# Optimization experiments

Hardware: AMD Instinct MI355X
Metric: run time of the kernel (lower is better)

## Reference

```python
import jax, jax.numpy as jnp
import numpy as np

B, T, C = 64, 384, 256
NH, NKV = 4, 2
HD = C // NH            # 64
NREP = NH // NKV        # 2
NE, TOPK = 8, 2
HID = int(8 / 3 * C)    # 682
EPS_RMS = 1e-6


def _rope_tables(t_len):
    inv_freq = 1.0 / (10000.0 ** (np.arange(0, HD, 2, dtype=np.float32) / HD))
    t = np.arange(t_len, dtype=np.float32)
    freqs = np.outer(t, inv_freq)                      # [T, HD/2]
    emb = np.concatenate([freqs, freqs], axis=-1)      # [T, HD]
    return jnp.asarray(np.cos(emb)), jnp.asarray(np.sin(emb))


def _rotate_half(x):
    h = x.shape[-1] // 2
    return jnp.concatenate([-x[..., h:], x[..., :h]], axis=-1)


def _rmsnorm(v, w):
    return v * jax.lax.rsqrt(jnp.mean(v * v, axis=-1, keepdims=True) + EPS_RMS) * w


def setup_inputs() -> dict:
    key = jax.random.key(0)
    ks = jax.random.split(key, 10)
    s = lambda k, shape: (jax.random.normal(k, shape, jnp.float32) * 0.02)
    return {
        "x": jax.random.normal(ks[0], (B, T, C), jnp.float32),
        "ln1_w": jnp.ones((C,), jnp.float32),
        "ln2_w": jnp.ones((C,), jnp.float32),
        "wq": s(ks[1], (NH * HD, C)),
        "wk": s(ks[2], (NKV * HD, C)),
        "wv": s(ks[3], (NKV * HD, C)),
        "wo": s(ks[4], (C, C)),
        "router_w": s(ks[5], (NE, C)),
        "w1": s(ks[6], (NE, HID, C)),
        "w2": s(ks[7], (NE, C, HID)),
        "w3": s(ks[8], (NE, HID, C)),
    }


def reference(x, ln1_w, ln2_w, wq, wk, wv, wo, router_w, w1, w2, w3):
    Bx, Tx, Cx = x.shape
    # --- attention sub-block ---
    h = _rmsnorm(x, ln1_w)
    q = (h @ wq.T).reshape(Bx, Tx, NH, HD).transpose(0, 2, 1, 3)    # [B,H,T,D]
    k = (h @ wk.T).reshape(Bx, Tx, NKV, HD).transpose(0, 2, 1, 3)   # [B,KV,T,D]
    v = (h @ wv.T).reshape(Bx, Tx, NKV, HD).transpose(0, 2, 1, 3)
    cos, sin = _rope_tables(Tx)
    cos, sin = cos[None, None], sin[None, None]
    q = q * cos + _rotate_half(q) * sin
    k = k * cos + _rotate_half(k) * sin
    k = jnp.repeat(k, NREP, axis=1)   # GQA: expand kv heads
    v = jnp.repeat(v, NREP, axis=1)
    scores = jnp.einsum('bhtd,bhsd->bhts', q, k) / jnp.sqrt(jnp.float32(HD))
    causal = jnp.tril(jnp.ones((Tx, Tx), dtype=bool))
    scores = jnp.where(causal[None, None], scores, jnp.float32(-1e30))
    att = jax.nn.softmax(scores, axis=-1)
    y = jnp.einsum('bhts,bhsd->bhtd', att, v).transpose(0, 2, 1, 3).reshape(Bx, Tx, Cx)
    x = x + y @ wo.T

    # --- MoE sub-block ---
    flat = _rmsnorm(x, ln2_w).reshape(-1, Cx)                  # [N, C]
    probs = jax.nn.softmax(flat @ router_w.T, axis=-1)         # [N, NE]
    tp, ti = jax.lax.top_k(probs, TOPK)
    tp = tp / (jnp.sum(tp, axis=-1, keepdims=True) + 1e-9)
    # per-token per-expert combine weight (0 if not selected)
    weights = jnp.sum(tp[..., None] * jax.nn.one_hot(ti, NE, dtype=flat.dtype), axis=1)  # [N, NE]
    out = jnp.zeros_like(flat)
    for e in range(NE):  # small fixed expert count
        hh = jax.nn.silu(flat @ w1[e].T) * (flat @ w3[e].T)
        out = out + weights[:, e:e + 1] * (hh @ w2[e].T)
    return x + out.reshape(Bx, Tx, Cx)
```

## Files before the change

kernel.cpp:

```cpp
#include <hip/hip_runtime.h>
#include <hip/hip_bf16.h>
#include <math.h>

typedef unsigned short u16t;
typedef __bf16 bf16x8 __attribute__((ext_vector_type(8)));
typedef float f32x4 __attribute__((ext_vector_type(4)));

#define NBATCH 64
#define NT 384
#define NC 256
#define NHID 682
#define NHIDP 704
#define NTOK (NBATCH * NT)
#define NSLOT (2 * NTOK + 1024)

#define SB0 196
#define SB1 (SB0 + 512)
#define SB2 (SB1 + 256)
#define SB3 (SB2 + 5632)
#define SB4 (SB3 + 5632)
#define SB5 (SB4 + 48)

static __device__ __forceinline__ float bf2f(u16t u) { return __uint_as_float(((unsigned int)u) << 16); }
static __device__ __forceinline__ u16t f2bf(float f) { return __builtin_bit_cast(u16t, __float2bfloat16(f)); }

static __device__ __forceinline__ void gload16(const void* gp, void* lp) {
  __builtin_amdgcn_global_load_lds((const __attribute__((address_space(1))) void*)gp,
                                   (__attribute__((address_space(3))) void*)lp, 16, 0, 0);
}

static __device__ __forceinline__ void pipe_barrier_full() {
  asm volatile("s_waitcnt vmcnt(0) lgkmcnt(0)" ::: "memory");
  __builtin_amdgcn_s_barrier();
  asm volatile("" ::: "memory");
}


__global__ __launch_bounds__(256) void k_setup(const float* __restrict__ wq, const float* __restrict__ wk,
                                               const float* __restrict__ wv, const float* __restrict__ wo,
                                               const float* __restrict__ w1, const float* __restrict__ w2,
                                               const float* __restrict__ w3,
                                               int* __restrict__ tok, float* __restrict__ tokw,
                                               int* __restrict__ ctrl,
                                               u16t* __restrict__ wqkvb, u16t* __restrict__ wob,
                                               u16t* __restrict__ w1p, u16t* __restrict__ w3p,
                                               u16t* __restrict__ w2p, float* __restrict__ rtab) {
  int blk = blockIdx.x, t = threadIdx.x;
  if (blk < SB0) {
    int i = blk * 256 + t;
    tok[i] = -1; tokw[i] = 0.f;
    if (blk == 0 && t < 64) ctrl[t] = 0;
  } else if (blk < SB1) {
    int i = (blk - SB0) * 256 + t;
    int row = i >> 8, col = i & 255;
    float s = (row < 256) ? wq[(size_t)row * 256 + col]
            : (row < 384) ? wk[(size_t)(row - 256) * 256 + col]
                          : wv[(size_t)(row - 384) * 256 + col];
    wqkvb[i] = f2bf(s);
  } else if (blk < SB2) {
    int i = (blk - SB1) * 256 + t;
    wob[i] = f2bf(wo[i]);
  } else if (blk < SB3) {
    int idx = (blk - SB2) * 256 + t;
    int kcol = idx & 255; int tmp = idx >> 8; int nrow = tmp % NHIDP; int e = tmp / NHIDP;
    if (nrow < NHID) {
      size_t src = ((size_t)e * NHID + nrow) * NC + kcol;
      w1p[idx] = f2bf(w1[src]); w3p[idx] = f2bf(w3[src]);
    } else { w1p[idx] = 0; w3p[idx] = 0; }
  } else if (blk < SB4) {
    int idx = (blk - SB3) * 256 + t;
    int kcol = idx % NHIDP; int tmp = idx / NHIDP; int nrow = tmp & 255; int e = tmp >> 8;
    w2p[idx] = (kcol < NHID) ? f2bf(w2[((size_t)e * NC + nrow) * NHID + kcol]) : (u16t)0;
  } else {
    int i = (blk - SB4) * 256 + t;
    int tt = i >> 5, d = i & 31;
    float ang = (float)tt * powf(10000.f, -(float)d * (1.f / 32.f));
    float s, c; sincosf(ang, &s, &c);
    ((float2*)rtab)[i] = make_float2(c, s);
  }
}

__global__ __launch_bounds__(256) void k_rms(const float* __restrict__ xin,
                                             const float* __restrict__ wg,
                                             u16t* __restrict__ out) {
  int w = threadIdx.x >> 6, l = threadIdx.x & 63;
  int n = blockIdx.x * 4 + w;
  const float* xr = xin + (size_t)n * NC;
  float4 xa = *(const float4*)(xr + l * 4);
  float ssq = xa.x * xa.x + xa.y * xa.y + xa.z * xa.z + xa.w * xa.w;
  for (int d = 1; d < 64; d <<= 1) ssq += __shfl_xor(ssq, d, 64);
  float rs = rsqrtf(ssq * (1.f / 256.f) + 1e-6f);
  float4 wa = *(const float4*)(wg + l * 4);
  ushort4 o;
  o.x = f2bf(xa.x * rs * wa.x);
  o.y = f2bf(xa.y * rs * wa.y);
  o.z = f2bf(xa.z * rs * wa.z);
  o.w = f2bf(xa.w * rs * wa.w);
  *(ushort4*)(out + (size_t)n * NC + l * 4) = o;
}

__global__ __launch_bounds__(256) void k_rms_router(const float* __restrict__ xin,
                                                    const float* __restrict__ wg,
                                                    const float* __restrict__ rw,
                                                    u16t* __restrict__ flat,
                                                    int* __restrict__ eidx,
                                                    float* __restrict__ ew) {
  int w = threadIdx.x >> 6, l = threadIdx.x & 63;
  int n = blockIdx.x * 4 + w;
  const float* xr = xin + (size_t)n * NC;
  float4 xa = *(const float4*)(xr + l * 4);
  float ssq = xa.x * xa.x + xa.y * xa.y + xa.z * xa.z + xa.w * xa.w;
  for (int d = 1; d < 64; d <<= 1) ssq += __shfl_xor(ssq, d, 64);
  float rs = rsqrtf(ssq * (1.f / 256.f) + 1e-6f);
  float4 wa = *(const float4*)(wg + l * 4);
  float n0 = xa.x * rs * wa.x, n1 = xa.y * rs * wa.y;
  float n2 = xa.z * rs * wa.z, n3 = xa.w * rs * wa.w;
  ushort4 o; o.x = f2bf(n0); o.y = f2bf(n1); o.z = f2bf(n2); o.w = f2bf(n3);
  *(ushort4*)(flat + (size_t)n * NC + l * 4) = o;
  float acc[8];
  for (int e = 0; e < 8; e++) {
    float4 ra = *(const float4*)(rw + (size_t)e * NC + l * 4);
    acc[e] = n0 * ra.x + n1 * ra.y + n2 * ra.z + n3 * ra.w;
  }
  for (int e = 0; e < 8; e++)
    for (int d = 1; d < 64; d <<= 1) acc[e] += __shfl_xor(acc[e], d, 64);
  if (l == 0) {
    float mx = acc[0];
    for (int e = 1; e < 8; e++) mx = fmaxf(mx, acc[e]);
    float p[8], sum = 0.f;
    for (int e = 0; e < 8; e++) { p[e] = __expf(acc[e] - mx); sum += p[e]; }
    float inv = 1.f / sum;
    for (int e = 0; e < 8; e++) p[e] *= inv;
    int i0 = 0; float b0 = p[0];
    for (int e = 1; e < 8; e++) if (p[e] > b0) { b0 = p[e]; i0 = e; }
    int i1 = -1; float b1 = -1.f;
    for (int e = 0; e < 8; e++) if (e != i0 && p[e] > b1) { b1 = p[e]; i1 = e; }
    float s2 = 1.f / (b0 + b1 + 1e-9f);
    eidx[n * 2] = i0; eidx[n * 2 + 1] = i1;
    ew[n * 2] = b0 * s2; ew[n * 2 + 1] = b1 * s2;
  }
}

__global__ __launch_bounds__(256) void k_hist(const int* __restrict__ eidx, int* __restrict__ ctrl) {
  int* cnt = ctrl; int* offs = ctrl + 8; int* cursor = ctrl + 20; int* done = ctrl + 32;
  __shared__ int lh[8];
  if (threadIdx.x < 8) lh[threadIdx.x] = 0;
  __syncthreads();
  int base = blockIdx.x * 1024 + threadIdx.x;
  for (int i = 0; i < 4; i++) atomicAdd(&lh[eidx[base + i * 256]], 1);
  __syncthreads();
  if (threadIdx.x < 8) {
    atomicAdd(&cnt[threadIdx.x], lh[threadIdx.x]);
    __threadfence();
  }
  __syncthreads();
  if (threadIdx.x == 0) {
    int prev = atomicAdd(done, 1);
    if (prev == 47) {
      int off = 0;
      for (int e = 0; e < 8; e++) {
        int c_ = atomicAdd(&cnt[e], 0);
        offs[e] = off; cursor[e] = off;
        off += ((c_ + 127) >> 7) << 7;
      }
      offs[8] = off;
    }
  }
}

__global__ __launch_bounds__(256) void k_gemm_qkv(const u16t* __restrict__ A,
                                                  const u16t* __restrict__ Bw,
                                                  const float* __restrict__ rtab,
                                                  u16t* __restrict__ qkv) {
  __shared__ __align__(16) u16t sA[2][128 * 64];
  __shared__ __align__(16) u16t sB[2][128 * 64];
  int t = threadIdx.x;
  int m0 = blockIdx.y * 128, n0 = blockIdx.x * 128;
  int w = t >> 6, l = t & 63, quad = l >> 4, lq = l & 15;
  int wm = (w >> 1) * 64, wn = (w & 1) * 64;
  const u16t* aP[4]; const u16t* bP[4];
  for (int i = 0; i < 4; i++) {
    int c = i * 256 + t; int r = c >> 3; int g = (c & 7) ^ (r & 7);
    aP[i] = A + (size_t)(m0 + r) * NC + g * 8;
    bP[i] = Bw + (size_t)(n0 + r) * NC + g * 8;
  }
  auto stage = [&](int p, int k0) {
    for (int i = 0; i < 4; i++) {
      gload16(aP[i] + k0, sA[p] + (size_t)(i * 256 + t) * 8);
      gload16(bP[i] + k0, sB[p] + (size_t)(i * 256 + t) * 8);
    }
  };
  const f32x4 fz = {0.f, 0.f, 0.f, 0.f};
  f32x4 acc[4][4];
  for (int i = 0; i < 4; i++) for (int j = 0; j < 4; j++) acc[i][j] = fz;
  stage(0, 0);
  pipe_barrier_full();
  for (int kb = 0; kb < 4; kb++) {
    int p = kb & 1;
    if (kb < 3) stage(p ^ 1, (kb + 1) << 6);
    for (int kk = 0; kk < 2; kk++) {
      int gq = kk * 4 + quad;
      bf16x8 af[4], bf[4];
      for (int mi = 0; mi < 4; mi++) { int row = wm + mi * 16 + lq; af[mi] = *(const bf16x8*)(sA[p] + (row * 8 + (gq ^ (row & 7))) * 8); }
      for (int ni = 0; ni < 4; ni++) { int row = wn + ni * 16 + lq; bf[ni] = *(const bf16x8*)(sB[p] + (row * 8 + (gq ^ (row & 7))) * 8); }
      for (int mi = 0; mi < 4; mi++)
        for (int ni = 0; ni < 4; ni++)
          acc[mi][ni] = __builtin_amdgcn_mfma_f32_16x16x32_bf16(af[mi], bf[ni], acc[mi][ni], 0, 0, 0);
    }
    if (kb < 3) pipe_barrier_full();
  }
  int cb = (n0 + wn) >> 6;
  const float2* rt = (const float2*)rtab;
  for (int mi = 0; mi < 4; mi++)
    for (int r = 0; r < 4; r++) {
      int gm = m0 + wm + mi * 16 + quad * 4 + r;
      u16t* orow = qkv + (size_t)gm * 512 + n0 + wn;
      if (cb < 6) {
        int tt = gm % NT;
        for (int ni = 0; ni < 2; ni++) {
          int d = ni * 16 + lq;
          float2 cs = rt[tt * 32 + d];
          float x1 = acc[mi][ni][r], x2 = acc[mi][ni + 2][r];
          orow[d] = f2bf(x1 * cs.x - x2 * cs.y);
          orow[d + 32] = f2bf(x2 * cs.x + x1 * cs.y);
        }
      } else {
        for (int ni = 0; ni < 4; ni++) orow[ni * 16 + lq] = f2bf(acc[mi][ni][r]);
      }
    }
}

__global__ __launch_bounds__(256) void k_gemm_wo(const u16t* __restrict__ A,
                                                 const u16t* __restrict__ Bw,
                                                 const float* __restrict__ xin,
                                                 float* __restrict__ xo) {
  __shared__ __align__(16) u16t sA[2][128 * 64];
  __shared__ __align__(16) u16t sB[2][128 * 64];
  int t = threadIdx.x;
  int m0 = blockIdx.y * 128, n0 = blockIdx.x * 128;
  int w = t >> 6, l = t & 63, quad = l >> 4, lq = l & 15;
  int wm = (w >> 1) * 64, wn = (w & 1) * 64;
  const u16t* aP[4]; const u16t* bP[4];
  for (int i = 0; i < 4; i++) {
    int c = i * 256 + t; int r = c >> 3; int g = (c & 7) ^ (r & 7);
    aP[i] = A + (size_t)(m0 + r) * NC + g * 8;
    bP[i] = Bw + (size_t)(n0 + r) * NC + g * 8;
  }
  auto stage = [&](int p, int k0) {
    for (int i = 0; i < 4; i++) {
      gload16(aP[i] + k0, sA[p] + (size_t)(i * 256 + t) * 8);
      gload16(bP[i] + k0, sB[p] + (size_t)(i * 256 + t) * 8);
    }
  };
  const f32x4 fz = {0.f, 0.f, 0.f, 0.f};
  f32x4 acc[4][4];
  for (int i = 0; i < 4; i++) for (int j = 0; j < 4; j++) acc[i][j] = fz;
  stage(0, 0);
  pipe_barrier_full();
  for (int kb = 0; kb < 4; kb++) {
    int p = kb & 1;
    if (kb < 3) stage(p ^ 1, (kb + 1) << 6);
    for (int kk = 0; kk < 2; kk++) {
      int gq = kk * 4 + quad;
      bf16x8 af[4], bf[4];
      for (int mi = 0; mi < 4; mi++) { int row = wm + mi * 16 + lq; af[mi] = *(const bf16x8*)(sA[p] + (row * 8 + (gq ^ (row & 7))) * 8); }
      for (int ni = 0; ni < 4; ni++) { int row = wn + ni * 16 + lq; bf[ni] = *(const bf16x8*)(sB[p] + (row * 8 + (gq ^ (row & 7))) * 8); }
      for (int mi = 0; mi < 4; mi++)
        for (int ni = 0; ni < 4; ni++)
          acc[mi][ni] = __builtin_amdgcn_mfma_f32_16x16x32_bf16(af[mi], bf[ni], acc[mi][ni], 0, 0, 0);
    }
    if (kb < 3) pipe_barrier_full();
  }
  for (int mi = 0; mi < 4; mi++)
    for (int ni = 0; ni < 4; ni++) {
      int gn = n0 + wn + ni * 16 + lq;
      for (int r = 0; r < 4; r++) {
        int gm = m0 + wm + mi * 16 + quad * 4 + r;
        xo[(size_t)gm * NC + gn] = acc[mi][ni][r] + xin[(size_t)gm * NC + gn];
      }
    }
}

__global__ __launch_bounds__(256) void k_attn(const u16t* __restrict__ qkv,
                                              u16t* __restrict__ y) {
  __shared__ __align__(16) u16t sK[2][64 * 64];
  __shared__ __align__(16) u16t sVT[2][64 * 64];
  __shared__ __align__(16) u16t sP[4 * 32 * 64];
  int qt = blockIdx.x, h = blockIdx.y, b = blockIdx.z;
  int kvh = h >> 1;
  int t = threadIdx.x, w = t >> 6, l = t & 63, quad = l >> 4, lq = l & 15;
  int tb = qt * 128 + w * 32;
  bf16x8 qf[2][2];
  for (int mi = 0; mi < 2; mi++)
    for (int kk = 0; kk < 2; kk++)
      qf[mi][kk] = *(const bf16x8*)(qkv + ((size_t)(b * NT + tb + mi * 16 + lq)) * 512 + h * 64 + kk * 32 + quad * 8);
  const f32x4 fz = {0.f, 0.f, 0.f, 0.f};
  f32x4 accO[2][4];
  float mrow[2][4], lrow[2][4];
  for (int mi = 0; mi < 2; mi++)
    for (int ni = 0; ni < 4; ni++) accO[mi][ni] = fz;
  for (int mi = 0; mi < 2; mi++)
    for (int r = 0; r < 4; r++) { mrow[mi][r] = -1e30f; lrow[mi][r] = 0.f; }
  u16t* myP = sP + w * 2048;
  int nkt = (qt + 1) * 2;
  ushort4 vr0[2], vr1[2];
  auto stageK = [&](int p, int kt) {
    int s0 = kt * 64;
    for (int i = 0; i < 2; i++) {
      int c = i * 256 + t; int s = c >> 3; int g = (c & 7) ^ (s & 7);
      gload16(qkv + ((size_t)(b * NT + s0 + s)) * 512 + 256 + kvh * 64 + g * 8, sK[p] + (size_t)c * 8);
    }
  };
  auto vload = [&](int kt) {
    int s0 = kt * 64;
    for (int i = 0; i < 2; i++) {
      int pI = i * 256 + t; int s = pI & 63; int n0 = (pI >> 6) * 8;
      const u16t* vp = qkv + ((size_t)(b * NT + s0 + s)) * 512 + 384 + kvh * 64 + n0;
      vr0[i] = *(const ushort4*)vp; vr1[i] = *(const ushort4*)(vp + 4);
    }
  };
  auto vstore = [&](int p) {
    for (int i = 0; i < 2; i++) {
      int pI = i * 256 + t; int s = pI & 63; int n0 = (pI >> 6) * 8;
      u16t vv[8] = {vr0[i].x, vr0[i].y, vr0[i].z, vr0[i].w, vr1[i].x, vr1[i].y, vr1[i].z, vr1[i].w};
      for (int j = 0; j < 8; j++) {
        int nn = n0 + j;
        sVT[p][(nn * 8 + ((s >> 3) ^ (nn & 7))) * 8 + (s & 7)] = vv[j];
      }
    }
  };
  stageK(0, 0); vload(0); vstore(0);
  pipe_barrier_full();
  for (int kt = 0; kt < nkt; kt++) {
    int p = kt & 1;
    int s0 = kt * 64;
    bool more = (kt + 1 < nkt);
    if (more) { stageK(p ^ 1, kt + 1); vload(kt + 1); }
    if (s0 <= tb + 31) {
      f32x4 accS[2][4];
      for (int mi = 0; mi < 2; mi++) for (int ni = 0; ni < 4; ni++) accS[mi][ni] = fz;
      for (int kk = 0; kk < 2; kk++) {
        int gq = kk * 4 + quad;
        bf16x8 kf[4];
        for (int ni = 0; ni < 4; ni++) { int row = ni * 16 + lq; kf[ni] = *(const bf16x8*)(sK[p] + (row * 8 + (gq ^ (row & 7))) * 8); }
        for (int mi = 0; mi < 2; mi++)
          for (int ni = 0; ni < 4; ni++)
            accS[mi][ni] = __builtin_amdgcn_mfma_f32_16x16x32_bf16(qf[mi][kk], kf[ni], accS[mi][ni], 0, 0, 0);
      }
      for (int mi = 0; mi < 2; mi++) {
        float alpha[4];
        for (int r = 0; r < 4; r++) {
          int trow = tb + mi * 16 + quad * 4 + r;
          float mx = -1e30f;
          for (int ni = 0; ni < 4; ni++) {
            int ss = s0 + ni * 16 + lq;
            float sv = accS[mi][ni][r] * 0.125f;
            sv = (ss > trow) ? -1e30f : sv;
            accS[mi][ni][r] = sv;
            mx = fmaxf(mx, sv);
          }
          for (int d = 1; d < 16; d <<= 1) mx = fmaxf(mx, __shfl_xor(mx, d, 64));
          float mnew = fmaxf(mrow[mi][r], mx);
          float al = __expf(mrow[mi][r] - mnew);
          float rsum = 0.f;
          for (int ni = 0; ni < 4; ni++) {
            float p2 = __expf(accS[mi][ni][r] - mnew);
            accS[mi][ni][r] = p2;
            rsum += p2;
          }
          for (int d = 1; d < 16; d <<= 1) rsum += __shfl_xor(rsum, d, 64);
          lrow[mi][r] = lrow[mi][r] * al + rsum;
          mrow[mi][r] = mnew;
          alpha[r] = al;
        }
        for (int ni = 0; ni < 4; ni++)
          for (int r = 0; r < 4; r++) accO[mi][ni][r] *= alpha[r];
        for (int ni = 0; ni < 4; ni++) {
          int cc = ni * 16 + lq;
          for (int r = 0; r < 4; r++) {
            int row = mi * 16 + quad * 4 + r;
            myP[((cc >> 3) * 32 + row) * 8 + (cc & 7)] = f2bf(accS[mi][ni][r]);
          }
        }
      }
      asm volatile("s_waitcnt lgkmcnt(0)" ::: "memory");
      for (int kk = 0; kk < 2; kk++) {
        int gq = kk * 4 + quad;
        bf16x8 pf[2], vf[4];
        for (int mi = 0; mi < 2; mi++) { int row = mi * 16 + lq; pf[mi] = *(const bf16x8*)(myP + (gq * 32 + row) * 8); }
        for (int ni = 0; ni < 4; ni++) { int row = ni * 16 + lq; vf[ni] = *(const bf16x8*)(sVT[p] + (row * 8 + (gq ^ (row & 7))) * 8); }
        for (int mi = 0; mi < 2; mi++)
          for (int ni = 0; ni < 4; ni++)
            accO[mi][ni] = __builtin_amdgcn_mfma_f32_16x16x32_bf16(pf[mi], vf[ni], accO[mi][ni], 0, 0, 0);
      }
    }
    if (more) {
      vstore(p ^ 1);
      pipe_barrier_full();
    }
  }
  for (int mi = 0; mi < 2; mi++)
    for (int r = 0; r < 4; r++) {
      int trow = tb + mi * 16 + quad * 4 + r;
      float inv = 1.f / lrow[mi][r];
      for (int ni = 0; ni < 4; ni++) {
        int d = ni * 16 + lq;
        y[((size_t)(b * NT + trow)) * NC + h * 64 + d] = f2bf(accO[mi][ni][r] * inv);
      }
    }
}

__global__ __launch_bounds__(256) void k_scatter(const int* __restrict__ eidx, const float* __restrict__ ew,
                                                 int* __restrict__ cursor, int* __restrict__ tok,
                                                 float* __restrict__ tokw, int* __restrict__ t2s) {
  __shared__ int lcnt[8], lbase[8];
  if (threadIdx.x < 8) lcnt[threadIdx.x] = 0;
  __syncthreads();
  int n = blockIdx.x * 256 + threadIdx.x;
  int e0 = eidx[n * 2], e1 = eidx[n * 2 + 1];
  int p0 = atomicAdd(&lcnt[e0], 1);
  int p1 = atomicAdd(&lcnt[e1], 1);
  __syncthreads();
  if (threadIdx.x < 8) lbase[threadIdx.x] = atomicAdd(&cursor[threadIdx.x], lcnt[threadIdx.x]);
  __syncthreads();
  int g0 = lbase[e0] + p0, g1 = lbase[e1] + p1;
  tok[g0] = n; tokw[g0] = ew[n * 2];
  tok[g1] = n; tokw[g1] = ew[n * 2 + 1];
  t2s[n * 2] = g0; t2s[n * 2 + 1] = g1;
}

__global__ __launch_bounds__(256) void k_moe_e1(const u16t* __restrict__ flat,
                                                const u16t* __restrict__ w1p,
                                                const u16t* __restrict__ w3p,
                                                const int* __restrict__ offs,
                                                const int* __restrict__ tok,
                                                u16t* __restrict__ hh) {
  __shared__ __align__(16) u16t sA[2][128 * 64];
  __shared__ __align__(16) u16t sB1[2][64 * 64];
  __shared__ __align__(16) u16t sB3[2][64 * 64];
  int t = threadIdx.x;
  int bid = blockIdx.x;
  int work = (bid & 7) * 539 + (bid >> 3);
  int sb = work / 11;
  int slot0 = sb * 128, n0 = (work - sb * 11) * 64;
  int e = 7;
  for (int i = 0; i < 8; i++) { if (slot0 < offs[i + 1]) { e = i; break; } }
  const u16t* B1 = w1p + (size_t)e * NHIDP * NC;
  const u16t* B3 = w3p + (size_t)e * NHIDP * NC;
  int w = t >> 6, l = t & 63, quad = l >> 4, lq = l & 15;
  int wm = (w >> 1) * 64, wn = (w & 1) * 32;
  const u16t* aP[4]; const u16t* b1P[2]; const u16t* b3P[2];
  for (int i = 0; i < 4; i++) {
    int c = i * 256 + t; int r = c >> 3; int g = (c & 7) ^ (r & 7);
    int tk = tok[slot0 + r]; int row = (tk < 0) ? 0 : tk;
    aP[i] = flat + (size_t)row * NC + g * 8;
  }
  for (int i = 0; i < 2; i++) {
    int c = i * 256 + t; int r = c >> 3; int g = (c & 7) ^ (r & 7);
    b1P[i] = B1 + (size_t)(n0 + r) * NC + g * 8;
    b3P[i] = B3 + (size_t)(n0 + r) * NC + g * 8;
  }
  auto stage = [&](int p, int k0) {
    for (int i = 0; i < 4; i++)
      gload16(aP[i] + k0, sA[p] + (size_t)(i * 256 + t) * 8);
    for (int i = 0; i < 2; i++) {
      gload16(b1P[i] + k0, sB1[p] + (size_t)(i * 256 + t) * 8);
      gload16(b3P[i] + k0, sB3[p] + (size_t)(i * 256 + t) * 8);
    }
  };
  const f32x4 fz = {0.f, 0.f, 0.f, 0.f};
  f32x4 a1[4][2], a3[4][2];
  for (int i = 0; i < 4; i++) for (int j = 0; j < 2; j++) { a1[i][j] = fz; a3[i][j] = fz; }
  stage(0, 0);
  pipe_barrier_full();
  for (int kb = 0; kb < 4; kb++) {
    int p = kb & 1;
    if (kb < 3) stage(p ^ 1, (kb + 1) << 6);
    for (int kk = 0; kk < 2; kk++) {
      int gq = kk * 4 + quad;
      bf16x8 af[4], b1f[2], b3f[2];
      for (int mi = 0; mi < 4; mi++) { int row = wm + mi * 16 + lq; af[mi] = *(const bf16x8*)(sA[p] + (row * 8 + (gq ^ (row & 7))) * 8); }
      for (int ni = 0; ni < 2; ni++) {
        int row = wn + ni * 16 + lq;
        b1f[ni] = *(const bf16x8*)(sB1[p] + (row * 8 + (gq ^ (row & 7))) * 8);
        b3f[ni] = *(const bf16x8*)(sB3[p] + (row * 8 + (gq ^ (row & 7))) * 8);
      }
      for (int mi = 0; mi < 4; mi++)
        for (int ni = 0; ni < 2; ni++) {
          a1[mi][ni] = __builtin_amdgcn_mfma_f32_16x16x32_bf16(af[mi], b1f[ni], a1[mi][ni], 0, 0, 0);
          a3[mi][ni] = __builtin_amdgcn_mfma_f32_16x16x32_bf16(af[mi], b3f[ni], a3[mi][ni], 0, 0, 0);
        }
    }
    if (kb < 3) pipe_barrier_full();
  }
  for (int mi = 0; mi < 4; mi++)
    for (int ni = 0; ni < 2; ni++) {
      int gn = n0 + wn + ni * 16 + lq;
      for (int r = 0; r < 4; r++) {
        int slot = slot0 + wm + mi * 16 + quad * 4 + r;
        float v1 = a1[mi][ni][r], v3 = a3[mi][ni][r];
        float hv = v1 / (1.f + __expf(-v1)) * v3;
        hh[(size_t)slot * NHIDP + gn] = f2bf(hv);
      }
    }
}

__global__ __launch_bounds__(256) void k_moe_e2(const u16t* __restrict__ hh,
                                                const u16t* __restrict__ w2p,
                                                const int* __restrict__ offs,
                                                const float* __restrict__ tokw,
                                                u16t* __restrict__ eo) {
  __shared__ __align__(16) u16t sA[2][128 * 64];
  __shared__ __align__(16) u16t sB[2][128 * 64];
  int t = threadIdx.x;
  int bid = blockIdx.x;
  int work = (bid & 7) * 98 + (bid >> 3);
  int slot0 = (work >> 1) * 128, n0 = (work & 1) * 128;
  int e = 7;
  for (int i = 0; i < 8; i++) { if (slot0 < offs[i + 1]) { e = i; break; } }
  const u16t* Bw = w2p + (size_t)e * NC * NHIDP;
  int w = t >> 6, l = t & 63, quad = l >> 4, lq = l & 15;
  int wm = (w >> 1) * 64, wn = (w & 1) * 64;
  const u16t* aP[4]; const u16t* bP[4];
  for (int i = 0; i < 4; i++) {
    int c = i * 256 + t; int r = c >> 3; int g = (c & 7) ^ (r & 7);
    aP[i] = hh + (size_t)(slot0 + r) * NHIDP + g * 8;
    bP[i] = Bw + (size_t)(n0 + r) * NHIDP + g * 8;
  }
  auto stage = [&](int p, int k0) {
    for (int i = 0; i < 4; i++) {
      gload16(aP[i] + k0, sA[p] + (size_t)(i * 256 + t) * 8);
      gload16(bP[i] + k0, sB[p] + (size_t)(i * 256 + t) * 8);
    }
  };
  const f32x4 fz = {0.f, 0.f, 0.f, 0.f};
  f32x4 acc[4][4];
  for (int i = 0; i < 4; i++) for (int j = 0; j < 4; j++) acc[i][j] = fz;
  stage(0, 0);
  pipe_barrier_full();
  for (int kb = 0; kb < 11; kb++) {
    int p = kb & 1;
    if (kb < 10) stage(p ^ 1, (kb + 1) << 6);
    for (int kk = 0; kk < 2; kk++) {
      int gq = kk * 4 + quad;
      bf16x8 af[4], bf[4];
      for (int mi = 0; mi < 4; mi++) { int row = wm + mi * 16 + lq; af[mi] = *(const bf16x8*)(sA[p] + (row * 8 + (gq ^ (row & 7))) * 8); }
      for (int ni = 0; ni < 4; ni++) { int row = wn + ni * 16 + lq; bf[ni] = *(const bf16x8*)(sB[p] + (row * 8 + (gq ^ (row & 7))) * 8); }
      for (int mi = 0; mi < 4; mi++)
        for (int ni = 0; ni < 4; ni++)
          acc[mi][ni] = __builtin_amdgcn_mfma_f32_16x16x32_bf16(af[mi], bf[ni], acc[mi][ni], 0, 0, 0);
    }
    if (kb < 10) pipe_barrier_full();
  }
  for (int mi = 0; mi < 4; mi++)
    for (int r = 0; r < 4; r++) {
      int slot = slot0 + wm + mi * 16 + quad * 4 + r;
      float wgt = tokw[slot];
      for (int ni = 0; ni < 4; ni++) {
        int gn = n0 + wn + ni * 16 + lq;
        eo[(size_t)slot * NC + gn] = f2bf(wgt * acc[mi][ni][r]);
      }
    }
}

__global__ __launch_bounds__(256) void k_combine(const u16t* __restrict__ eo,
                                                 const int* __restrict__ t2s,
                                                 float* __restrict__ xo) {
  int w = threadIdx.x >> 6, l = threadIdx.x & 63;
  int n = blockIdx.x * 4 + w;
  int g0 = t2s[n * 2], g1 = t2s[n * 2 + 1];
  float* xr = xo + (size_t)n * NC + l * 4;
  float4 xa = *(const float4*)xr;
  ushort4 a = *(const ushort4*)(eo + (size_t)g0 * NC + l * 4);
  ushort4 b = *(const ushort4*)(eo + (size_t)g1 * NC + l * 4);
  xa.x += bf2f(a.x) + bf2f(b.x);
  xa.y += bf2f(a.y) + bf2f(b.y);
  xa.z += bf2f(a.z) + bf2f(b.z);
  xa.w += bf2f(a.w) + bf2f(b.w);
  *(float4*)xr = xa;
}

extern "C" void kernel_launch(void* const* d_in, const int* in_sizes, int n_in,
                              void* d_out, int out_size, void* d_ws, size_t ws_size,
                              hipStream_t stream) {
  (void)in_sizes; (void)n_in; (void)out_size; (void)ws_size;
  const float* x    = (const float*)d_in[0];
  const float* ln1w = (const float*)d_in[1];
  const float* ln2w = (const float*)d_in[2];
  const float* wq   = (const float*)d_in[3];
  const float* wk   = (const float*)d_in[4];
  const float* wv   = (const float*)d_in[5];
  const float* wo   = (const float*)d_in[6];
  const float* rw   = (const float*)d_in[7];
  const float* w1   = (const float*)d_in[8];
  const float* w2   = (const float*)d_in[9];
  const float* w3   = (const float*)d_in[10];
  float* xo = (float*)d_out;

  char* ws = (char*)d_ws;
  size_t off = 0;
  int* ctrl  = (int*)(ws + off);  off += 4096;
  int* eidx  = (int*)(ws + off);  off += (size_t)NTOK * 2 * 4;
  float* ew  = (float*)(ws + off); off += (size_t)NTOK * 2 * 4;
  int* tok   = (int*)(ws + off);  off += (size_t)NSLOT * 4;
  float* tokw = (float*)(ws + off); off += (size_t)NSLOT * 4;
  int* t2s   = (int*)(ws + off);  off += (size_t)NTOK * 2 * 4;
  u16t* wqkvb = (u16t*)(ws + off); off += (size_t)512 * 256 * 2;
  u16t* wob  = (u16t*)(ws + off); off += (size_t)256 * 256 * 2;
  u16t* w1p  = (u16t*)(ws + off); off += (size_t)8 * NHIDP * NC * 2;
  u16t* w3p  = (u16t*)(ws + off); off += (size_t)8 * NHIDP * NC * 2;
  u16t* w2p  = (u16t*)(ws + off); off += (size_t)8 * NC * NHIDP * 2;
  float* rtab = (float*)(ws + off); off += (size_t)NT * 32 * 2 * 4;
  u16t* h    = (u16t*)(ws + off); off += (size_t)NTOK * NC * 2;
  u16t* qkv  = (u16t*)(ws + off); off += (size_t)NTOK * 512 * 2;
  u16t* y    = (u16t*)(ws + off); off += (size_t)NTOK * NC * 2;
  u16t* flat = (u16t*)(ws + off); off += (size_t)NTOK * NC * 2;
  u16t* hh   = (u16t*)(ws + off); off += (size_t)NSLOT * NHIDP * 2;
  u16t* eo   = h;
  int* offs = ctrl + 8; int* cursor = ctrl + 20;

  k_setup<<<SB5, 256, 0, stream>>>(wq, wk, wv, wo, w1, w2, w3,
                                   tok, tokw, ctrl, wqkvb, wob, w1p, w3p, w2p, rtab);
  k_rms<<<NTOK / 4, 256, 0, stream>>>(x, ln1w, h);
  k_gemm_qkv<<<dim3(4, NTOK / 128), 256, 0, stream>>>(h, wqkvb, rtab, qkv);
  k_attn<<<dim3(3, 4, NBATCH), 256, 0, stream>>>(qkv, y);
  k_gemm_wo<<<dim3(2, NTOK / 128), 256, 0, stream>>>(y, wob, x, xo);

  k_rms_router<<<NTOK / 4, 256, 0, stream>>>(xo, ln2w, rw, flat, eidx, ew);
  k_hist<<<48, 256, 0, stream>>>(eidx, ctrl);
  k_scatter<<<NTOK / 256, 256, 0, stream>>>(eidx, ew, cursor, tok, tokw, t2s);
  k_moe_e1<<<4312, 256, 0, stream>>>(flat, w1p, w3p, offs, tok, hh);
  k_moe_e2<<<784, 256, 0, stream>>>(hh, w2p, offs, tokw, eo);
  k_combine<<<NTOK / 4, 256, 0, stream>>>(eo, t2s, xo);
}
```

Measured before the change: 306.7 us.

## Single-buffer MoE GEMM LDS, raise MFMA priority, fold first RMSNorm into setup

The two MoE expert GEMM kernels drop LDS double buffering. Each K step now loads, syncs, computes and syncs again, which halves shared memory per block so more blocks can be resident. MFMA sections are wrapped in s_setprio to favour math waves. The first RMSNorm is merged into the setup kernel as extra blocks, removing one launch. The trade-off is that global loads no longer overlap compute within a block, so the kernel relies on occupancy to hide latency.

```diff
diff --git a/kernel.cpp b/kernel.cpp
--- a/kernel.cpp
+++ b/kernel.cpp
@@ -20,6 +20,7 @@
 #define SB3 (SB2 + 5632)
 #define SB4 (SB3 + 5632)
 #define SB5 (SB4 + 48)
+#define SB6 (SB5 + NTOK / 4)
 
 static __device__ __forceinline__ float bf2f(u16t u) { return __uint_as_float(((unsigned int)u) << 16); }
 static __device__ __forceinline__ u16t f2bf(float f) { return __builtin_bit_cast(u16t, __float2bfloat16(f)); }
@@ -40,11 +41,13 @@
                                                const float* __restrict__ wv, const float* __restrict__ wo,
                                                const float* __restrict__ w1, const float* __restrict__ w2,
                                                const float* __restrict__ w3,
+                                               const float* __restrict__ x, const float* __restrict__ ln1w,
                                                int* __restrict__ tok, float* __restrict__ tokw,
                                                int* __restrict__ ctrl,
                                                u16t* __restrict__ wqkvb, u16t* __restrict__ wob,
                                                u16t* __restrict__ w1p, u16t* __restrict__ w3p,
-                                               u16t* __restrict__ w2p, float* __restrict__ rtab) {
+                                               u16t* __restrict__ w2p, float* __restrict__ rtab,
+                                               u16t* __restrict__ h) {
   int blk = blockIdx.x, t = threadIdx.x;
   if (blk < SB0) {
     int i = blk * 256 + t;
@@ -71,32 +74,28 @@
     int idx = (blk - SB3) * 256 + t;
     int kcol = idx % NHIDP; int tmp = idx / NHIDP; int nrow = tmp & 255; int e = tmp >> 8;
     w2p[idx] = (kcol < NHID) ? f2bf(w2[((size_t)e * NC + nrow) * NHID + kcol]) : (u16t)0;
-  } else {
+  } else if (blk < SB5) {
     int i = (blk - SB4) * 256 + t;
     int tt = i >> 5, d = i & 31;
     float ang = (float)tt * powf(10000.f, -(float)d * (1.f / 32.f));
     float s, c; sincosf(ang, &s, &c);
     ((float2*)rtab)[i] = make_float2(c, s);
-  }
-}
-
-__global__ __launch_bounds__(256) void k_rms(const float* __restrict__ xin,
-                                             const float* __restrict__ wg,
-                                             u16t* __restrict__ out) {
-  int w = threadIdx.x >> 6, l = threadIdx.x & 63;
-  int n = blockIdx.x * 4 + w;
-  const float* xr = xin + (size_t)n * NC;
-  float4 xa = *(const float4*)(xr + l * 4);
-  float ssq = xa.x * xa.x + xa.y * xa.y + xa.z * xa.z + xa.w * xa.w;
-  for (int d = 1; d < 64; d <<= 1) ssq += __shfl_xor(ssq, d, 64);
-  float rs = rsqrtf(ssq * (1.f / 256.f) + 1e-6f);
-  float4 wa = *(const float4*)(wg + l * 4);
-  ushort4 o;
-  o.x = f2bf(xa.x * rs * wa.x);
-  o.y = f2bf(xa.y * rs * wa.y);
-  o.z = f2bf(xa.z * rs * wa.z);
-  o.w = f2bf(xa.w * rs * wa.w);
-  *(ushort4*)(out + (size_t)n * NC + l * 4) = o;
+  } else {
+    int w = t >> 6, l = t & 63;
+    int n = (blk - SB5) * 4 + w;
+    const float* xr = x + (size_t)n * NC;
+    float4 xa = *(const float4*)(xr + l * 4);
+    float ssq = xa.x * xa.x + xa.y * xa.y + xa.z * xa.z + xa.w * xa.w;
+    for (int d = 1; d < 64; d <<= 1) ssq += __shfl_xor(ssq, d, 64);
+    float rs = rsqrtf(ssq * (1.f / 256.f) + 1e-6f);
+    float4 wa = *(const float4*)(ln1w + l * 4);
+    ushort4 o;
+    o.x = f2bf(xa.x * rs * wa.x);
+    o.y = f2bf(xa.y * rs * wa.y);
+    o.z = f2bf(xa.z * rs * wa.z);
+    o.w = f2bf(xa.w * rs * wa.w);
+    *(ushort4*)(h + (size_t)n * NC + l * 4) = o;
+  }
 }
 
 __global__ __launch_bounds__(256) void k_rms_router(const float* __restrict__ xin,
@@ -435,9 +434,9 @@
                                                 const int* __restrict__ offs,
                                                 const int* __restrict__ tok,
                                                 u16t* __restrict__ hh) {
-  __shared__ __align__(16) u16t sA[2][128 * 64];
-  __shared__ __align__(16) u16t sB1[2][64 * 64];
-  __shared__ __align__(16) u16t sB3[2][64 * 64];
+  __shared__ __align__(16) u16t sA[128 * 64];
+  __shared__ __align__(16) u16t sB1[64 * 64];
+  __shared__ __align__(16) u16t sB3[64 * 64];
   int t = threadIdx.x;
   int bid = blockIdx.x;
   int work = (bid & 7) * 539 + (bid >> 3);
@@ -460,38 +459,36 @@
     b1P[i] = B1 + (size_t)(n0 + r) * NC + g * 8;
     b3P[i] = B3 + (size_t)(n0 + r) * NC + g * 8;
   }
-  auto stage = [&](int p, int k0) {
-    for (int i = 0; i < 4; i++)
-      gload16(aP[i] + k0, sA[p] + (size_t)(i * 256 + t) * 8);
-    for (int i = 0; i < 2; i++) {
-      gload16(b1P[i] + k0, sB1[p] + (size_t)(i * 256 + t) * 8);
-      gload16(b3P[i] + k0, sB3[p] + (size_t)(i * 256 + t) * 8);
-    }
-  };
   const f32x4 fz = {0.f, 0.f, 0.f, 0.f};
   f32x4 a1[4][2], a3[4][2];
   for (int i = 0; i < 4; i++) for (int j = 0; j < 2; j++) { a1[i][j] = fz; a3[i][j] = fz; }
-  stage(0, 0);
-  pipe_barrier_full();
   for (int kb = 0; kb < 4; kb++) {
-    int p = kb & 1;
-    if (kb < 3) stage(p ^ 1, (kb + 1) << 6);
+    int k0 = kb << 6;
+    for (int i = 0; i < 4; i++)
+      gload16(aP[i] + k0, sA + (size_t)(i * 256 + t) * 8);
+    for (int i = 0; i < 2; i++) {
+      gload16(b1P[i] + k0, sB1 + (size_t)(i * 256 + t) * 8);
+      gload16(b3P[i] + k0, sB3 + (size_t)(i * 256 + t) * 8);
+    }
+    __syncthreads();
     for (int kk = 0; kk < 2; kk++) {
       int gq = kk * 4 + quad;
       bf16x8 af[4], b1f[2], b3f[2];
-      for (int mi = 0; mi < 4; mi++) { int row = wm + mi * 16 + lq; af[mi] = *(const bf16x8*)(sA[p] + (row * 8 + (gq ^ (row & 7))) * 8); }
+      for (int mi = 0; mi < 4; mi++) { int row = wm + mi * 16 + lq; af[mi] = *(const bf16x8*)(sA + (row * 8 + (gq ^ (row & 7))) * 8); }
       for (int ni = 0; ni < 2; ni++) {
         int row = wn + ni * 16 + lq;
-        b1f[ni] = *(const bf16x8*)(sB1[p] + (row * 8 + (gq ^ (row & 7))) * 8);
-        b3f[ni] = *(const bf16x8*)(sB3[p] + (row * 8 + (gq ^ (row & 7))) * 8);
-      }
+        b1f[ni] = *(const bf16x8*)(sB1 + (row * 8 + (gq ^ (row & 7))) * 8);
+        b3f[ni] = *(const bf16x8*)(sB3 + (row * 8 + (gq ^ (row & 7))) * 8);
+      }
+      __builtin_amdgcn_s_setprio(1);
       for (int mi = 0; mi < 4; mi++)
         for (int ni = 0; ni < 2; ni++) {
           a1[mi][ni] = __builtin_amdgcn_mfma_f32_16x16x32_bf16(af[mi], b1f[ni], a1[mi][ni], 0, 0, 0);
           a3[mi][ni] = __builtin_amdgcn_mfma_f32_16x16x32_bf16(af[mi], b3f[ni], a3[mi][ni], 0, 0, 0);
         }
-    }
-    if (kb < 3) pipe_barrier_full();
+      __builtin_amdgcn_s_setprio(0);
+    }
+    __syncthreads();
   }
   for (int mi = 0; mi < 4; mi++)
     for (int ni = 0; ni < 2; ni++) {
@@ -510,8 +507,8 @@
                                                 const int* __restrict__ offs,
                                                 const float* __restrict__ tokw,
                                                 u16t* __restrict__ eo) {
-  __shared__ __align__(16) u16t sA[2][128 * 64];
-  __shared__ __align__(16) u16t sB[2][128 * 64];
+  __shared__ __align__(16) u16t sA[128 * 64];
+  __shared__ __align__(16) u16t sB[128 * 64];
   int t = threadIdx.x;
   int bid = blockIdx.x;
   int work = (bid & 7) * 98 + (bid >> 3);
@@ -527,30 +524,28 @@
     aP[i] = hh + (size_t)(slot0 + r) * NHIDP + g * 8;
     bP[i] = Bw + (size_t)(n0 + r) * NHIDP + g * 8;
   }
-  auto stage = [&](int p, int k0) {
-    for (int i = 0; i < 4; i++) {
-      gload16(aP[i] + k0, sA[p] + (size_t)(i * 256 + t) * 8);
-      gload16(bP[i] + k0, sB[p] + (size_t)(i * 256 + t) * 8);
-    }
-  };
   const f32x4 fz = {0.f, 0.f, 0.f, 0.f};
   f32x4 acc[4][4];
   for (int i = 0; i < 4; i++) for (int j = 0; j < 4; j++) acc[i][j] = fz;
-  stage(0, 0);
-  pipe_barrier_full();
   for (int kb = 0; kb < 11; kb++) {
-    int p = kb & 1;
-    if (kb < 10) stage(p ^ 1, (kb + 1) << 6);
+    int k0 = kb << 6;
+    for (int i = 0; i < 4; i++) {
+      gload16(aP[i] + k0, sA + (size_t)(i * 256 + t) * 8);
+      gload16(bP[i] + k0, sB + (size_t)(i * 256 + t) * 8);
+    }
+    __syncthreads();
     for (int kk = 0; kk < 2; kk++) {
       int gq = kk * 4 + quad;
       bf16x8 af[4], bf[4];
-      for (int mi = 0; mi < 4; mi++) { int row = wm + mi * 16 + lq; af[mi] = *(const bf16x8*)(sA[p] + (row * 8 + (gq ^ (row & 7))) * 8); }
-      for (int ni = 0; ni < 4; ni++) { int row = wn + ni * 16 + lq; bf[ni] = *(const bf16x8*)(sB[p] + (row * 8 + (gq ^ (row & 7))) * 8); }
+      for (int mi = 0; mi < 4; mi++) { int row = wm + mi * 16 + lq; af[mi] = *(const bf16x8*)(sA + (row * 8 + (gq ^ (row & 7))) * 8); }
+      for (int ni = 0; ni < 4; ni++) { int row = wn + ni * 16 + lq; bf[ni] = *(const bf16x8*)(sB + (row * 8 + (gq ^ (row & 7))) * 8); }
+      __builtin_amdgcn_s_setprio(1);
       for (int mi = 0; mi < 4; mi++)
         for (int ni = 0; ni < 4; ni++)
           acc[mi][ni] = __builtin_amdgcn_mfma_f32_16x16x32_bf16(af[mi], bf[ni], acc[mi][ni], 0, 0, 0);
-    }
-    if (kb < 10) pipe_barrier_full();
+      __builtin_amdgcn_s_setprio(0);
+    }
+    __syncthreads();
   }
   for (int mi = 0; mi < 4; mi++)
     for (int r = 0; r < 4; r++) {
@@ -619,9 +614,8 @@
   u16t* eo   = h;
   int* offs = ctrl + 8; int* cursor = ctrl + 20;
 
-  k_setup<<<SB5, 256, 0, stream>>>(wq, wk, wv, wo, w1, w2, w3,
-                                   tok, tokw, ctrl, wqkvb, wob, w1p, w3p, w2p, rtab);
-  k_rms<<<NTOK / 4, 256, 0, stream>>>(x, ln1w, h);
+  k_setup<<<SB6, 256, 0, stream>>>(wq, wk, wv, wo, w1, w2, w3, x, ln1w,
+                                   tok, tokw, ctrl, wqkvb, wob, w1p, w3p, w2p, rtab, h);
   k_gemm_qkv<<<dim3(4, NTOK / 128), 256, 0, stream>>>(h, wqkvb, rtab, qkv);
   k_attn<<<dim3(3, 4, NBATCH), 256, 0, stream>>>(qkv, y);
   k_gemm_wo<<<dim3(2, NTOK / 128), 256, 0, stream>>>(y, wob, x, xo);
```

Result: no change. 301.4 us (-1.7%).
